# Kernel tuning notes

Hardware: AMD Instinct MI355X
Metric: run time of the kernel (lower is better)

Reference implementation:

```python
import jax, jax.numpy as jnp
import numpy as np

B, T, IN, D, H, L, OUT = 256, 100, 6, 1024, 8, 4, 256
HD = D // H
SCALE = 1.0 / float(np.sqrt(HD))


def _pe(t, d):
    # sinusoidal positional encoding [t, d]
    pos = np.arange(t, dtype=np.float32)[:, None]
    div = np.exp(np.arange(0, d, 2, dtype=np.float32) * (-np.log(10000.0) / d))
    pe = np.zeros((t, d), np.float32)
    pe[:, 0::2] = np.sin(pos * div)
    pe[:, 1::2] = np.cos(pos * div)
    return jnp.asarray(pe)


def _ln(x, g, b, eps=1e-5):
    m = x.mean(-1, keepdims=True)
    v = ((x - m) ** 2).mean(-1, keepdims=True)
    return (x - m) * jax.lax.rsqrt(v + eps) * g + b


def setup_inputs() -> dict:
    ks = jax.random.split(jax.random.key(0), 8)
    s = 0.02
    return {
        "x": jax.random.normal(ks[0], (B, T, IN), jnp.float32),
        "Wi": jax.random.normal(ks[1], (IN, D), jnp.float32) * s,
        "bi": jnp.zeros((D,), jnp.float32),
        "qkv_w": jax.random.normal(ks[2], (L, 3 * D, D), jnp.float32) * s,
        "qkv_b": jnp.zeros((L, 3 * D), jnp.float32),
        "out_w": jax.random.normal(ks[3], (L, D, D), jnp.float32) * s,
        "out_b": jnp.zeros((L, D), jnp.float32),
        "ff1_w": jax.random.normal(ks[4], (L, D, D), jnp.float32) * s,
        "ff1_b": jnp.zeros((L, D), jnp.float32),
        "ff2_w": jax.random.normal(ks[5], (L, D, D), jnp.float32) * s,
        "ff2_b": jnp.zeros((L, D), jnp.float32),
        "ln1_g": jnp.ones((L, D), jnp.float32),
        "ln1_b": jnp.zeros((L, D), jnp.float32),
        "ln2_g": jnp.ones((L, D), jnp.float32),
        "ln2_b": jnp.zeros((L, D), jnp.float32),
        "Wo": jax.random.normal(ks[6], (T * D, OUT), jnp.float32) * s,
        "bo": jnp.zeros((OUT,), jnp.float32),
    }


def reference(x, Wi, bi, qkv_w, qkv_b, out_w, out_b, ff1_w, ff1_b,
              ff2_w, ff2_b, ln1_g, ln1_b, ln2_g, ln2_b, Wo, bo):
    b, t, _ = x.shape
    # vectorized equivalent of the python double loop: mask[i, j, :] = 1 where x[i, j, 0] == 0
    row = (x[:, :, 0] == 0).astype(x.dtype)                    # [B, T]
    base = jnp.broadcast_to(row[:, :, None], (b, t, t))        # [B, T, T]
    # torch: mask.repeat(H,1,1).reshape(H*B, T, T); MHA batch slot (bi, h) reads flat b*H+h
    amask = jnp.tile(base, (H, 1, 1)).reshape(b, H, t, t)      # additive float mask (+1)

    h = x @ Wi + bi + _pe(t, D)[None, :, :]                     # [B, T, D] (dropout off at eval)

    for i in range(L):  # post-norm encoder layers, identical weights structure
        qkv = h @ qkv_w[i].T + qkv_b[i]
        q, k, v = jnp.split(qkv, 3, axis=-1)
        q = q.reshape(b, t, H, HD)
        k = k.reshape(b, t, H, HD)
        v = v.reshape(b, t, H, HD)
        scores = jnp.einsum('bqhd,bkhd->bhqk', q, k) * SCALE + amask
        attn = jax.nn.softmax(scores, axis=-1)
        ctx = jnp.einsum('bhqk,bkhd->bqhd', attn, v).reshape(b, t, D)
        h = _ln(h + ctx @ out_w[i].T + out_b[i], ln1_g[i], ln1_b[i])
        ff = jax.nn.relu(h @ ff1_w[i].T + ff1_b[i]) @ ff2_w[i].T + ff2_b[i]
        h = _ln(h + ff, ln2_g[i], ln2_b[i])

    return h.reshape(b, t * D) @ Wo + bo                        # [B, OUT]
```

## Files before the change

### kernel.cpp

```cpp
#include <hip/hip_runtime.h>


#define B_    256
#define T_    100
#define D_    1024
#define H_    8
#define HD_   128
#define L_    4
#define BT_   25600
#define DQ_   3072
#define OUT_  256
#define KFIN_ 102400
#define KSPLIT_ 32
#define SCALE_ 0.08838834764831845f

typedef unsigned short ushort_t;
typedef __attribute__((ext_vector_type(8))) short bf16x8;
typedef __attribute__((ext_vector_type(4))) float f32x4;

__device__ inline ushort_t f2bf(float f) {
  unsigned u = __float_as_uint(f);
  u += 0x7FFFu + ((u >> 16) & 1u);
  return (ushort_t)(u >> 16);
}
__device__ inline float bf2f(ushort_t u) {
  return __uint_as_float((unsigned)u << 16);
}

__device__ inline void gld16(const void* g, void* l) {
  __builtin_amdgcn_global_load_lds(
      (__attribute__((address_space(1))) unsigned int*)(size_t)g,
      (__attribute__((address_space(3))) unsigned int*)l, 16, 0, 0);
}

#define GBUF_ 65536
#define GBOF_ 32768

#define STAGE256(hs_) do { \
    const int hs__ = (hs_); \
    if (hs__ < 64) { \
      const int tt__ = hs__ >> 2, id__ = hs__ & 3; \
      const int half__ = id__ >> 1; \
      const int bo__ = (tt__ & 1) * GBUF_ + half__ * 16384 + wsl \
                     + ((id__ & 1) ? GBOF_ : 0); \
      const ushort_t* s__ = ((id__ & 1) ? gB : gA) \
                     + (size_t)(half__ * 128) * 1024 + tt__ * 64; \
      gld16(s__, lds + bo__); \
      gld16(s__ + 8 * 1024, lds + bo__ + 1024); \
    } \
  } while (0)

#define LDA256(Mi) do { \
    const char* ba__ = lds + ldsoff + (Mi) * 16384 + rbA; \
    _Pragma("unroll") for (int i_ = 0; i_ < 4; ++i_) { \
      aF[i_][0] = *(const bf16x8*)(ba__ + i_ * 2048 + c0); \
      aF[i_][1] = *(const bf16x8*)(ba__ + i_ * 2048 + c1); \
    } \
  } while (0)

#define LDB256(Ni, BF) do { \
    const char* bb__ = lds + ldsoff + (Ni) * 16384 + rbB; \
    _Pragma("unroll") for (int j_ = 0; j_ < 2; ++j_) { \
      BF[j_][0] = *(const bf16x8*)(bb__ + j_ * 2048 + c0); \
      BF[j_][1] = *(const bf16x8*)(bb__ + j_ * 2048 + c1); \
    } \
  } while (0)

#define MM256(Mi, Ni, BF) do { \
    _Pragma("unroll") for (int i_ = 0; i_ < 4; ++i_) \
      _Pragma("unroll") for (int j_ = 0; j_ < 2; ++j_) { \
        acc[Mi][Ni][i_][j_] = __builtin_amdgcn_mfma_f32_16x16x32_bf16( \
            aF[i_][0], BF[j_][0], acc[Mi][Ni][i_][j_], 0, 0, 0); \
        acc[Mi][Ni][i_][j_] = __builtin_amdgcn_mfma_f32_16x16x32_bf16( \
            aF[i_][1], BF[j_][1], acc[Mi][Ni][i_][j_], 0, 0, 0); \
      } \
  } while (0)

#define VM6_ asm volatile("s_waitcnt vmcnt(6)" ::: "memory")
#define VM0_ asm volatile("s_waitcnt vmcnt(0)" ::: "memory")

#define PH256(t, p, LOADS, Mi, Ni, BF, VM) do { \
    LOADS; \
    STAGE256(7 + 4 * (t) + (p)); \
    __builtin_amdgcn_s_barrier(); \
    asm volatile("s_waitcnt lgkmcnt(0)" ::: "memory"); \
    __builtin_amdgcn_sched_barrier(0); \
    __builtin_amdgcn_s_setprio(1); \
    MM256(Mi, Ni, BF); \
    __builtin_amdgcn_s_setprio(0); \
    VM; \
    __builtin_amdgcn_s_barrier(); \
  } while (0)

#define TILE256(t, VM) do { \
    const int ldsoff = ((t) & 1) * GBUF_; \
    PH256(t, 0, { LDA256(0); LDB256(0, bF0); }, 0, 0, bF0, (void)0); \
    PH256(t, 1, { LDB256(1, bF1); },            0, 1, bF1, (void)0); \
    PH256(t, 2, { LDA256(1); },                 1, 1, bF1, (void)0); \
    PH256(t, 3, { },                            1, 0, bF0, VM); \
  } while (0)

template<int RELU, int RESID>
__global__ __launch_bounds__(512, 1)
void gemm256(const ushort_t* __restrict__ A, const ushort_t* __restrict__ Bw,
             const float* __restrict__ bias,
             ushort_t* __restrict__ outb, const ushort_t* __restrict__ resid,
             int N)
{
  __shared__ char lds[131072];
  const int tid = threadIdx.x;
  const int lane = tid & 63, w = tid >> 6;
  const int fr = lane & 15, q = lane >> 4;
  const int wm = w >> 2, wn = w & 3;

  const int nwg = gridDim.x;
  const int nbx = N >> 8;
  const int qd = nwg >> 3, r8 = nwg & 7;
  const int xcd = blockIdx.x & 7, idx = blockIdx.x >> 3;
  const int wg = (xcd < r8 ? xcd * (qd + 1) : r8 * (qd + 1) + (xcd - r8) * qd) + idx;
  const int m0 = (wg / nbx) * 256, n0 = (wg % nbx) * 256;

  const int lr8 = lane >> 3;
  const int xch = (lane & 7) ^ lr8;
  const ushort_t* gA = A  + (size_t)(m0 + w * 16 + lr8) * 1024 + xch * 8;
  const ushort_t* gB = Bw + (size_t)(n0 + w * 16 + lr8) * 1024 + xch * 8;
  const int wsl = w * 2048;

  const int c0 = (q ^ (fr & 7)) * 16;
  const int c1 = ((4 + q) ^ (fr & 7)) * 16;
  const int rbA = (wm * 64 + fr) * 128;
  const int rbB = GBOF_ + (wn * 32 + fr) * 128;

  f32x4 acc[2][2][4][2];
  #pragma unroll
  for (int a0 = 0; a0 < 2; ++a0)
    #pragma unroll
    for (int a1 = 0; a1 < 2; ++a1)
      #pragma unroll
      for (int a2 = 0; a2 < 4; ++a2)
        #pragma unroll
        for (int a3 = 0; a3 < 2; ++a3) acc[a0][a1][a2][a3] = 0.f;
  bf16x8 aF[4][2], bF0[2][2], bF1[2][2];

  #pragma unroll
  for (int hs = 0; hs < 7; ++hs) STAGE256(hs);
  VM6_;
  __builtin_amdgcn_s_barrier();

  for (int tp = 0; tp < 7; ++tp) {
    TILE256(2 * tp,     VM6_);
    TILE256(2 * tp + 1, VM6_);
  }
  TILE256(14, VM0_);
  TILE256(15, (void)0);

  const int erow = lane >> 2;
  const int ecc  = lane & 3;
  char* wb = lds + w * 4096;
  float bvv[2][2];
  #pragma unroll
  for (int Ni = 0; Ni < 2; ++Ni)
    #pragma unroll
    for (int jn = 0; jn < 2; ++jn)
      bvv[Ni][jn] = bias ? bias[n0 + Ni * 128 + wn * 32 + jn * 16 + fr] : 0.f;

  #pragma unroll
  for (int Mi = 0; Mi < 2; ++Mi)
    #pragma unroll
    for (int Ni = 0; Ni < 2; ++Ni) {
      #pragma unroll
      for (int i = 0; i < 4; ++i)
        #pragma unroll
        for (int jn = 0; jn < 2; ++jn)
          #pragma unroll
          for (int rr = 0; rr < 4; ++rr) {
            const int row = i * 16 + q * 4 + rr;
            float v = acc[Mi][Ni][i][jn][rr] + bvv[Ni][jn];
            if (RELU) v = fmaxf(v, 0.f);
            const int cp = (jn * 2 + (fr >> 3)) ^ ((row >> 2) & 3);
            *(ushort_t*)(wb + row * 64 + cp * 16 + (fr & 7) * 2) = f2bf(v);
          }
      #pragma unroll
      for (int rd = 0; rd < 4; ++rd) {
        const int row = rd * 16 + erow;
        const int sc = ecc ^ ((row >> 2) & 3);
        bf16x8 seg = *(const bf16x8*)(wb + row * 64 + sc * 16);
        const size_t gaddr = (size_t)(m0 + Mi * 128 + wm * 64 + row) * N
                           + (n0 + Ni * 128 + wn * 32 + ecc * 8);
        if (RESID) {
          const bf16x8 rv = *(const bf16x8*)&resid[gaddr];
          #pragma unroll
          for (int e = 0; e < 8; ++e)
            seg[e] = (short)f2bf(bf2f((ushort_t)seg[e]) + bf2f((ushort_t)rv[e]));
        }
        *(bf16x8*)&outb[gaddr] = seg;
      }
    }
}

template<int RELU, int RESID, int OBF, int OF32>
__global__ __launch_bounds__(256)
void gemm_nt(const ushort_t* __restrict__ A, const ushort_t* __restrict__ Bw,
             const float* __restrict__ bias,
             ushort_t* outb, float* outf, const ushort_t* __restrict__ resid,
             int M, int N, int K, int ksteps)
{
  __shared__ ushort_t lds[16384];
  ushort_t* lsA = lds;
  ushort_t* lsB = lds + 8192;
  const int tid = threadIdx.x, lane = tid & 63, wave = tid >> 6;
  const int fr = lane & 15, q = lane >> 4;
  const int m0 = blockIdx.y * 128, n0 = blockIdx.x * 128;
  const int wm = (wave >> 1) * 64, wn = (wave & 1) * 64;
  const int kbase = blockIdx.z * ksteps * 64;

  const ushort_t* Ab = A + (size_t)m0 * K + kbase;
  const ushort_t* Bb = Bw + (size_t)n0 * K + kbase;

  const int kg = (lane & 7) ^ (lane >> 3);
  const ushort_t* gaA = Ab + (size_t)(lane >> 3) * K + kg * 8;
  const ushort_t* gaB = Bb + (size_t)(lane >> 3) * K + kg * 8;

  f32x4 acc[4][4];
  #pragma unroll
  for (int i = 0; i < 4; i++)
    #pragma unroll
    for (int j = 0; j < 4; j++) acc[i][j] = 0.f;

  int rowA[4], rowB[4];
  #pragma unroll
  for (int t = 0; t < 4; t++) {
    rowA[t] = (wm + t * 16 + fr) * 64;
    rowB[t] = (wn + t * 16 + fr) * 64;
  }
  const int sl0 = ((0 * 4 + q) ^ (fr & 7)) * 8;
  const int sl1 = ((1 * 4 + q) ^ (fr & 7)) * 8;

  for (int ks = 0; ks < ksteps; ks++) {
    __syncthreads();
    #pragma unroll
    for (int u = 0; u < 4; u++) {
      const int i = wave * 4 + u;
      gld16(gaA + ks * 64 + (size_t)i * 8 * K, lsA + i * 512);
      gld16(gaB + ks * 64 + (size_t)i * 8 * K, lsB + i * 512);
    }
    __syncthreads();
    #pragma unroll
    for (int s = 0; s < 2; s++) {
      const int sl = s ? sl1 : sl0;
      bf16x8 af[4], bfv[4];
      #pragma unroll
      for (int t = 0; t < 4; t++) {
        af[t]  = *(const bf16x8*)(lsA + rowA[t] + sl);
        bfv[t] = *(const bf16x8*)(lsB + rowB[t] + sl);
      }
      #pragma unroll
      for (int i = 0; i < 4; i++)
        #pragma unroll
        for (int j = 0; j < 4; j++)
          acc[i][j] = __builtin_amdgcn_mfma_f32_16x16x32_bf16(af[i], bfv[j], acc[i][j], 0, 0, 0);
    }
  }

  if (OBF) {
    __syncthreads();
    ushort_t* myl = lds + wave * 2048;
    const int rloc = lane >> 2, cg = lane & 3;
    #pragma unroll
    for (int hh = 0; hh < 2; hh++) {
      #pragma unroll
      for (int j2 = 0; j2 < 2; j2++) {
        const int j = 2 * hh + j2;
        const float bv = bias ? bias[n0 + wn + j * 16 + fr] : 0.f;
        #pragma unroll
        for (int i = 0; i < 4; i++) {
          #pragma unroll
          for (int rr = 0; rr < 4; rr++) {
            const int row = i * 16 + q * 4 + rr;
            const int col = j2 * 16 + fr;
            float v = acc[i][j][rr] + bv;
            if (RELU) v = fmaxf(v, 0.f);
            const int cgw = col >> 3, cwi = col & 7;
            myl[(row * 4 + (cgw ^ (row & 3) ^ ((row >> 2) & 3))) * 8 + cwi] = f2bf(v);
          }
        }
      }
      #pragma unroll
      for (int rb = 0; rb < 4; rb++) {
        const int row = rb * 16 + rloc;
        const int cgr = cg ^ (row & 3) ^ ((row >> 2) & 3);
        bf16x8 seg = *(const bf16x8*)&myl[(row * 4 + cgr) * 8];
        const size_t gaddr = (size_t)(m0 + wm + row) * N + (n0 + wn + hh * 32 + cg * 8);
        if (RESID) {
          const bf16x8 rv = *(const bf16x8*)&resid[gaddr];
          #pragma unroll
          for (int e = 0; e < 8; e++) {
            const float f = bf2f((ushort_t)seg[e]) + bf2f((ushort_t)rv[e]);
            seg[e] = (short)f2bf(f);
          }
        }
        *(bf16x8*)&outb[gaddr] = seg;
      }
    }
  }
  if (OF32) {
    float* po = outf + (size_t)blockIdx.z * M * N;
    #pragma unroll
    for (int i = 0; i < 4; i++) {
      const int rb = m0 + wm + i * 16 + q * 4;
      #pragma unroll
      for (int j = 0; j < 4; j++) {
        const int col = n0 + wn + j * 16 + fr;
        #pragma unroll
        for (int rr = 0; rr < 4; rr++)
          po[(size_t)(rb + rr) * N + col] = acc[i][j][rr];
      }
    }
  }
}

#define KST 136
#define VST 120
#define PST 120

__global__ __launch_bounds__(256)
void attn_kernel(const ushort_t* __restrict__ qkv, ushort_t* __restrict__ ctx)
{
  __shared__ ushort_t Kls[112 * KST];
  __shared__ ushort_t Vt[128 * VST];
  __shared__ ushort_t Pls[64 * PST];
  const int tid = threadIdx.x, lane = tid & 63, wave = tid >> 6;
  const int fr = lane & 15, q = lane >> 4;
  const int hh = blockIdx.x, bb = blockIdx.y;
  const size_t base = (size_t)bb * T_ * DQ_;
  const ushort_t* Qb = qkv + base + hh * HD_;
  const ushort_t* Kb = qkv + base + D_ + hh * HD_;
  const ushort_t* Vb = qkv + base + 2 * D_ + hh * HD_;

  for (int e = tid; e < 1600; e += 256) {
    const int j = e >> 4, kc = e & 15;
    *(bf16x8*)&Kls[j * KST + kc * 8] = *(const bf16x8*)(Kb + (size_t)j * DQ_ + kc * 8);
  }
  for (int e = tid; e < 12 * KST; e += 256) Kls[100 * KST + e] = 0;
  for (int e = tid; e < 1600; e += 256) {
    const int j = e >> 4, dc = e & 15;
    const bf16x8 v = *(const bf16x8*)(Vb + (size_t)j * DQ_ + dc * 8);
    #pragma unroll
    for (int u = 0; u < 8; u++) Vt[(dc * 8 + u) * VST + j] = (ushort_t)v[u];
  }
  for (int e = tid; e < 128 * 12; e += 256) {
    const int d = e / 12, j = e - d * 12;
    Vt[d * VST + 100 + j] = 0;
  }
  __syncthreads();

  for (int c = 0; c < 2; c++) {
    if (c) __syncthreads();
    const int it  = c * 4 + wave;
    const bool wlive = (it < 7);
    const int itc = wlive ? it : 6;
    const int qrow = min(itc * 16 + fr, T_ - 1);
    bf16x8 aq[4];
    #pragma unroll
    for (int ks = 0; ks < 4; ks++)
      aq[ks] = *(const bf16x8*)(Qb + (size_t)qrow * DQ_ + ks * 32 + q * 8);
    f32x4 sacc[7];
    #pragma unroll
    for (int jt = 0; jt < 7; jt++) sacc[jt] = 0.f;
    #pragma unroll
    for (int ks = 0; ks < 4; ks++) {
      const int kk = ks * 32 + q * 8;
      #pragma unroll
      for (int jt = 0; jt < 7; jt++) {
        const bf16x8 kb = *(const bf16x8*)&Kls[(jt * 16 + fr) * KST + kk];
        sacc[jt] = __builtin_amdgcn_mfma_f32_16x16x32_bf16(aq[ks], kb, sacc[jt], 0, 0, 0);
      }
    }
    ushort_t pbf[7][4];
    #pragma unroll
    for (int rr = 0; rr < 4; rr++) {
      float sv[7];
      float mx = -1e30f;
      #pragma unroll
      for (int jt = 0; jt < 7; jt++) {
        float s = sacc[jt][rr] * SCALE_;
        if (jt == 6 && fr >= 4) s = -1e30f;
        sv[jt] = s;
        mx = fmaxf(mx, s);
      }
      mx = fmaxf(mx, __shfl_xor(mx, 1));
      mx = fmaxf(mx, __shfl_xor(mx, 2));
      mx = fmaxf(mx, __shfl_xor(mx, 4));
      mx = fmaxf(mx, __shfl_xor(mx, 8));
      float sum = 0.f;
      #pragma unroll
      for (int jt = 0; jt < 7; jt++) { sv[jt] = __expf(sv[jt] - mx); sum += sv[jt]; }
      sum += __shfl_xor(sum, 1);
      sum += __shfl_xor(sum, 2);
      sum += __shfl_xor(sum, 4);
      sum += __shfl_xor(sum, 8);
      const float inv = 1.f / sum;
      #pragma unroll
      for (int jt = 0; jt < 7; jt++) pbf[jt][rr] = f2bf(sv[jt] * inv);
    }
    if (wlive) {
      #pragma unroll
      for (int jt = 0; jt < 7; jt++)
        #pragma unroll
        for (int rr = 0; rr < 4; rr++)
          Pls[(wave * 16 + q * 4 + rr) * PST + jt * 16 + fr] = pbf[jt][rr];
    }
    __syncthreads();
    const int mtc = (c == 0) ? 4 : 3;
    f32x4 cacc[4][2];
    #pragma unroll
    for (int i = 0; i < 4; i++) { cacc[i][0] = 0.f; cacc[i][1] = 0.f; }
    #pragma unroll
    for (int ks = 0; ks < 4; ks++) {
      const int kk = ks * 32 + q * 8;
      const bool live = (ks < 3) || (q < 2);
      bf16x8 v0 = 0, v1 = 0;
      if (live) {
        v0 = *(const bf16x8*)&Vt[((wave * 2 + 0) * 16 + fr) * VST + kk];
        v1 = *(const bf16x8*)&Vt[((wave * 2 + 1) * 16 + fr) * VST + kk];
      }
      for (int mt = 0; mt < mtc; mt++) {
        bf16x8 a = 0;
        if (live) a = *(const bf16x8*)&Pls[(mt * 16 + fr) * PST + kk];
        cacc[mt][0] = __builtin_amdgcn_mfma_f32_16x16x32_bf16(a, v0, cacc[mt][0], 0, 0, 0);
        cacc[mt][1] = __builtin_amdgcn_mfma_f32_16x16x32_bf16(a, v1, cacc[mt][1], 0, 0, 0);
      }
    }
    for (int mt = 0; mt < mtc; mt++) {
      #pragma unroll
      for (int nn = 0; nn < 2; nn++) {
        const int col = hh * HD_ + (wave * 2 + nn) * 16 + fr;
        #pragma unroll
        for (int rr = 0; rr < 4; rr++) {
          const int r = c * 64 + mt * 16 + q * 4 + rr;
          if (r < T_)
            ctx[(size_t)(bb * T_ + r) * D_ + col] = f2bf(cacc[mt][nn][rr]);
        }
      }
    }
  }
}

__global__ __launch_bounds__(256)
void ln_kernel(const ushort_t* __restrict__ in, ushort_t* __restrict__ outb,
               const float* __restrict__ g, const float* __restrict__ bta)
{
  const int row = blockIdx.x, tid = threadIdx.x;
  const int c4 = tid * 4;
  const ushort4 uv = *(const ushort4*)(in + (size_t)row * D_ + c4);
  const float v0 = bf2f(uv.x), v1 = bf2f(uv.y), v2 = bf2f(uv.z), v3 = bf2f(uv.w);
  float s  = v0 + v1 + v2 + v3;
  float ss = v0*v0 + v1*v1 + v2*v2 + v3*v3;
  #pragma unroll
  for (int o = 1; o < 64; o <<= 1) {
    s  += __shfl_xor(s, o);
    ss += __shfl_xor(ss, o);
  }
  __shared__ float red[8];
  const int lane = tid & 63, wave = tid >> 6;
  if (lane == 0) { red[wave] = s; red[4 + wave] = ss; }
  __syncthreads();
  s  = red[0] + red[1] + red[2] + red[3];
  ss = red[4] + red[5] + red[6] + red[7];
  const float mean = s * (1.f / D_);
  const float var  = ss * (1.f / D_) - mean * mean;
  const float rstd = rsqrtf(var + 1e-5f);
  const float4 gv = *(const float4*)(g + c4);
  const float4 bv = *(const float4*)(bta + c4);
  ushort4 ob = { f2bf((v0 - mean) * rstd * gv.x + bv.x),
                 f2bf((v1 - mean) * rstd * gv.y + bv.y),
                 f2bf((v2 - mean) * rstd * gv.z + bv.z),
                 f2bf((v3 - mean) * rstd * gv.w + bv.w) };
  *(ushort4*)(outb + (size_t)row * D_ + c4) = ob;
}

__global__ __launch_bounds__(256)
void pe_init(float* __restrict__ pe)
{
  const int t = blockIdx.x;
  #pragma unroll
  for (int j = 0; j < 2; ++j) {
    const int k = threadIdx.x + j * 256;
    const float ang = (float)t * expf((float)k * -0.017988946039015984f);
    float s, c;
    sincosf(ang, &s, &c);
    pe[t * D_ + 2 * k]     = s;
    pe[t * D_ + 2 * k + 1] = c;
  }
}

__global__ __launch_bounds__(256)
void embed_kernel(const float* __restrict__ x, const float* __restrict__ Wi,
                  const float* __restrict__ bi, const float* __restrict__ pe,
                  ushort_t* __restrict__ hbf)
{
  const int row = blockIdx.x;
  const int t = row % T_;
  const int c = threadIdx.x * 4;
  float xv[6];
  #pragma unroll
  for (int i = 0; i < 6; i++) xv[i] = x[row * 6 + i];
  const float4 pv = *(const float4*)(pe + t * D_ + c);
  const float4 bv = *(const float4*)(bi + c);
  float a0 = bv.x + pv.x, a1 = bv.y + pv.y, a2 = bv.z + pv.z, a3 = bv.w + pv.w;
  #pragma unroll
  for (int i = 0; i < 6; i++) {
    const float4 wv = *(const float4*)(Wi + i * D_ + c);
    a0 += xv[i] * wv.x; a1 += xv[i] * wv.y;
    a2 += xv[i] * wv.z; a3 += xv[i] * wv.w;
  }
  ushort4 ob = { f2bf(a0), f2bf(a1), f2bf(a2), f2bf(a3) };
  *(ushort4*)(hbf + (size_t)row * D_ + c) = ob;
}

#define NQW (L_*DQ_*D_)
#define NDW (L_*D_*D_)
__global__ void cvt_all(const float* __restrict__ qw, const float* __restrict__ ow,
                        const float* __restrict__ f1, const float* __restrict__ f2,
                        ushort_t* wq, ushort_t* wo, ushort_t* w1, ushort_t* w2)
{
  const size_t i = ((size_t)blockIdx.x * 256 + threadIdx.x) * 4;
  const float* s; ushort_t* d; size_t off;
  if (i < NQW)                { s = qw; d = wq; off = i; }
  else if (i < NQW + NDW)     { s = ow; d = wo; off = i - NQW; }
  else if (i < NQW + 2*NDW)   { s = f1; d = w1; off = i - NQW - NDW; }
  else                        { s = f2; d = w2; off = i - NQW - 2*NDW; }
  const float4 v = *(const float4*)(s + off);
  ushort4 o = { f2bf(v.x), f2bf(v.y), f2bf(v.z), f2bf(v.w) };
  *(ushort4*)(d + off) = o;
}

__global__ __launch_bounds__(256)
void transpose_wo(const float* __restrict__ src, ushort_t* __restrict__ dst)
{
  __shared__ float tile[64][65];
  const int k0 = blockIdx.x * 64, n0 = blockIdx.y * 64;
  const int tc = threadIdx.x & 63, tr = threadIdx.x >> 6;
  #pragma unroll
  for (int i = 0; i < 16; i++) {
    const int r = i * 4 + tr;
    tile[r][tc] = src[(size_t)(k0 + r) * OUT_ + n0 + tc];
  }
  __syncthreads();
  #pragma unroll
  for (int i = 0; i < 16; i++) {
    const int n = i * 4 + tr;
    dst[(size_t)(n0 + n) * KFIN_ + k0 + tc] = f2bf(tile[tc][n]);
  }
}

__global__ void reduce_final(const float* __restrict__ part,
                             const float* __restrict__ bo, float* __restrict__ out)
{
  const int i = blockIdx.x * 256 + threadIdx.x;
  float s = bo[i & (OUT_ - 1)];
  for (int z = 0; z < KSPLIT_; z++) s += part[(size_t)z * OUT_ * OUT_ + i];
  out[i] = s;
}

extern "C" void kernel_launch(void* const* d_in, const int* in_sizes, int n_in,
                              void* d_out, int out_size, void* d_ws, size_t ws_size,
                              hipStream_t stream)
{
  (void)in_sizes; (void)n_in; (void)out_size; (void)ws_size;
  const float* x     = (const float*)d_in[0];
  const float* Wi    = (const float*)d_in[1];
  const float* bi    = (const float*)d_in[2];
  const float* qkv_w = (const float*)d_in[3];
  const float* qkv_b = (const float*)d_in[4];
  const float* out_w = (const float*)d_in[5];
  const float* out_b = (const float*)d_in[6];
  const float* ff1_w = (const float*)d_in[7];
  const float* ff1_b = (const float*)d_in[8];
  const float* ff2_w = (const float*)d_in[9];
  const float* ff2_b = (const float*)d_in[10];
  const float* ln1_g = (const float*)d_in[11];
  const float* ln1_b = (const float*)d_in[12];
  const float* ln2_g = (const float*)d_in[13];
  const float* ln2_b = (const float*)d_in[14];
  const float* Wo    = (const float*)d_in[15];
  const float* bo    = (const float*)d_in[16];
  float* out = (float*)d_out;

  char* p = (char*)d_ws;
  ushort_t* hbf  = (ushort_t*)p; p += (size_t)BT_ * D_ * 2;
  ushort_t* qkvb = (ushort_t*)p; p += (size_t)BT_ * DQ_ * 2;
  ushort_t* ctxb = (ushort_t*)p; p += (size_t)BT_ * D_ * 2;
  ushort_t* wq   = (ushort_t*)p; p += (size_t)NQW * 2;
  ushort_t* wo   = (ushort_t*)p; p += (size_t)NDW * 2;
  ushort_t* w1   = (ushort_t*)p; p += (size_t)NDW * 2;
  ushort_t* w2   = (ushort_t*)p; p += (size_t)NDW * 2;
  float*    pe   = (float*)p;    p += (size_t)T_ * D_ * 4;
  ushort_t* ffact = qkvb;
  ushort_t* sum   = qkvb + (size_t)BT_ * D_;
  ushort_t* wot   = ctxb;
  float*    part  = (float*)qkvb;

  cvt_all<<<dim3((NQW + 3*NDW) / 1024), 256, 0, stream>>>(
      qkv_w, out_w, ff1_w, ff2_w, wq, wo, w1, w2);
  pe_init<<<dim3(T_), 256, 0, stream>>>(pe);
  embed_kernel<<<dim3(BT_), 256, 0, stream>>>(x, Wi, bi, pe, hbf);

  for (int i = 0; i < L_; i++) {
    gemm256<0,0><<<dim3((BT_/256)*(DQ_/256)), 512, 0, stream>>>(
        hbf, wq + (size_t)i * DQ_ * D_, qkv_b + i * DQ_, qkvb, nullptr, DQ_);
    attn_kernel<<<dim3(H_, B_), 256, 0, stream>>>(qkvb, ctxb);
    gemm256<0,1><<<dim3((BT_/256)*(D_/256)), 512, 0, stream>>>(
        ctxb, wo + (size_t)i * D_ * D_, out_b + i * D_, sum, hbf, D_);
    ln_kernel<<<dim3(BT_), 256, 0, stream>>>(sum, hbf, ln1_g + i * D_, ln1_b + i * D_);
    gemm256<1,0><<<dim3((BT_/256)*(D_/256)), 512, 0, stream>>>(
        hbf, w1 + (size_t)i * D_ * D_, ff1_b + i * D_, ffact, nullptr, D_);
    gemm256<0,1><<<dim3((BT_/256)*(D_/256)), 512, 0, stream>>>(
        ffact, w2 + (size_t)i * D_ * D_, ff2_b + i * D_, sum, hbf, D_);
    ln_kernel<<<dim3(BT_), 256, 0, stream>>>(sum, hbf, ln2_g + i * D_, ln2_b + i * D_);
  }

  transpose_wo<<<dim3(KFIN_/64, OUT_/64), 256, 0, stream>>>(Wo, wot);
  gemm_nt<0,0,0,1><<<dim3(OUT_/128, OUT_/128, KSPLIT_), 256, 0, stream>>>(
      hbf, wot, nullptr, nullptr, part, nullptr,
      OUT_, OUT_, KFIN_, KFIN_ / (KSPLIT_ * 64));
  reduce_final<<<dim3(OUT_ * OUT_ / 256), 256, 0, stream>>>(part, bo, out);
}
```

Baseline: 2.373 ms.

## Add 128x256 double-buffered GEMM for D-by-D layers and unroll attention loops

Adds a new gemm128 kernel with 128x256 output tiles, a double-buffered LDS pipeline, XCD-aware block remapping and an occupancy hint of four workgroups. It replaces the 256x256 GEMM for the out-projection, FF1 and FF2 layers. For N=1024 the larger tiles gave only 400 workgroups, and the smaller tiles give 800, which spreads the work more evenly over the compute units. The attention kernel's PV and store loops are also fully unrolled with predication. The dead OBF epilogue is removed from gemm_nt. The risks are less data reuse per tile and heavier register pressure.

```diff
diff --git a/kernel.cpp b/kernel.cpp
--- a/kernel.cpp
+++ b/kernel.cpp
@@ -32,6 +32,12 @@
       (__attribute__((address_space(1))) unsigned int*)(size_t)g,
       (__attribute__((address_space(3))) unsigned int*)l, 16, 0, 0);
 }
+
+#define MFMA_(a, b, c) __builtin_amdgcn_mfma_f32_16x16x32_bf16(a, b, c, 0, 0, 0)
+
+#define VM6_ asm volatile("s_waitcnt vmcnt(6)" ::: "memory")
+#define VM3_ asm volatile("s_waitcnt vmcnt(3)" ::: "memory")
+#define VM0_ asm volatile("s_waitcnt vmcnt(0)" ::: "memory")
 
 #define GBUF_ 65536
 #define GBOF_ 32768
@@ -69,15 +75,10 @@
 #define MM256(Mi, Ni, BF) do { \
     _Pragma("unroll") for (int i_ = 0; i_ < 4; ++i_) \
       _Pragma("unroll") for (int j_ = 0; j_ < 2; ++j_) { \
-        acc[Mi][Ni][i_][j_] = __builtin_amdgcn_mfma_f32_16x16x32_bf16( \
-            aF[i_][0], BF[j_][0], acc[Mi][Ni][i_][j_], 0, 0, 0); \
-        acc[Mi][Ni][i_][j_] = __builtin_amdgcn_mfma_f32_16x16x32_bf16( \
-            aF[i_][1], BF[j_][1], acc[Mi][Ni][i_][j_], 0, 0, 0); \
+        acc[Mi][Ni][i_][j_] = MFMA_(aF[i_][0], BF[j_][0], acc[Mi][Ni][i_][j_]); \
+        acc[Mi][Ni][i_][j_] = MFMA_(aF[i_][1], BF[j_][1], acc[Mi][Ni][i_][j_]); \
       } \
   } while (0)
-
-#define VM6_ asm volatile("s_waitcnt vmcnt(6)" ::: "memory")
-#define VM0_ asm volatile("s_waitcnt vmcnt(0)" ::: "memory")
 
 #define PH256(t, p, LOADS, Mi, Ni, BF, VM) do { \
     LOADS; \
@@ -198,6 +199,132 @@
     }
 }
 
+#define LBUF_ 24576
+
+#define STG(t_) do { \
+    const int lo__ = ((t_) & 1) * LBUF_; \
+    gld16(gA  + (t_) * 32, lds + lo__ + dA); \
+    gld16(gB0 + (t_) * 32, lds + lo__ + dB0); \
+    gld16(gB1 + (t_) * 32, lds + lo__ + dB0 + 1024); \
+  } while (0)
+
+#define TIL(t_, STAGES_, VMW_) do { \
+    const int lo_ = ((t_) & 1) * LBUF_; \
+    _Pragma("unroll") for (int i_ = 0; i_ < 4; ++i_) \
+      aF[i_] = *(const bf16x8*)(lds + lo_ + rbA + i_ * 1024 + cR); \
+    _Pragma("unroll") for (int j_ = 0; j_ < 4; ++j_) \
+      bF[j_] = *(const bf16x8*)(lds + lo_ + rbB + j_ * 1024 + cR); \
+    asm volatile("s_waitcnt lgkmcnt(0)" ::: "memory"); \
+    __builtin_amdgcn_sched_barrier(0); \
+    __builtin_amdgcn_s_setprio(1); \
+    _Pragma("unroll") for (int i_ = 0; i_ < 4; ++i_) { \
+      acc[i_][0] = MFMA_(aF[i_], bF[0], acc[i_][0]); \
+      acc[i_][1] = MFMA_(aF[i_], bF[1], acc[i_][1]); } \
+    __builtin_amdgcn_s_setprio(0); \
+    __builtin_amdgcn_s_barrier(); \
+    __builtin_amdgcn_sched_barrier(0); \
+    STAGES_; \
+    __builtin_amdgcn_s_setprio(1); \
+    _Pragma("unroll") for (int i_ = 0; i_ < 4; ++i_) { \
+      acc[i_][2] = MFMA_(aF[i_], bF[2], acc[i_][2]); \
+      acc[i_][3] = MFMA_(aF[i_], bF[3], acc[i_][3]); } \
+    __builtin_amdgcn_s_setprio(0); \
+    VMW_; \
+    __builtin_amdgcn_s_barrier(); \
+    __builtin_amdgcn_sched_barrier(0); \
+  } while (0)
+
+template<int RELU, int RESID>
+__global__ __launch_bounds__(512, 4)
+void gemm128(const ushort_t* __restrict__ A, const ushort_t* __restrict__ Bw,
+             const float* __restrict__ bias,
+             ushort_t* __restrict__ outb, const ushort_t* __restrict__ resid,
+             int N)
+{
+  __shared__ __align__(16) char lds[49152];
+  const int tid = threadIdx.x;
+  const int lane = tid & 63, w = tid >> 6;
+  const int fr = lane & 15, q = lane >> 4;
+  const int wm = w >> 2, wn = w & 3;
+
+  const int nwg = gridDim.x;
+  const int nbx = N >> 8;
+  const int qd = nwg >> 3, r8 = nwg & 7;
+  const int xcd = blockIdx.x & 7, idx = blockIdx.x >> 3;
+  const int wg = (xcd < r8 ? xcd * (qd + 1) : r8 * (qd + 1) + (xcd - r8) * qd) + idx;
+  const int m0 = (wg / nbx) * 128, n0 = (wg % nbx) * 256;
+
+  const int xc = (lane & 3) ^ ((lane >> 3) & 3);
+  const ushort_t* gA  = A  + (size_t)(m0 + w * 16 + (lane >> 2)) * 1024 + xc * 8;
+  const ushort_t* gB0 = Bw + (size_t)(n0 + w * 32 + (lane >> 2)) * 1024 + xc * 8;
+  const ushort_t* gB1 = gB0 + 16 * 1024;
+  const int dA  = w * 1024;
+  const int dB0 = 8192 + w * 2048;
+
+  const int cR  = fr * 64 + ((q ^ ((fr >> 1) & 3)) << 4);
+  const int rbA = wm * 4096;
+  const int rbB = 8192 + wn * 4096;
+
+  f32x4 acc[4][4];
+  #pragma unroll
+  for (int i = 0; i < 4; ++i)
+    #pragma unroll
+    for (int j = 0; j < 4; ++j) acc[i][j] = 0.f;
+  bf16x8 aF[4], bF[4];
+
+  STG(0); STG(1);
+  VM3_;
+  __builtin_amdgcn_s_barrier();
+  __builtin_amdgcn_sched_barrier(0);
+
+  #pragma unroll
+  for (int t = 0; t < 30; ++t) TIL(t, STG(t + 2), VM3_);
+  TIL(30, (void)0, VM0_);
+  TIL(31, (void)0, (void)0);
+  __syncthreads();
+
+  const int erow = lane >> 2;
+  const int ecc  = lane & 3;
+  char* wb = lds + w * 4096;
+  float bvv[2][2];
+  #pragma unroll
+  for (int jh = 0; jh < 2; ++jh)
+    #pragma unroll
+    for (int jn = 0; jn < 2; ++jn)
+      bvv[jh][jn] = bias ? bias[n0 + wn * 64 + jh * 32 + jn * 16 + fr] : 0.f;
+
+  #pragma unroll
+  for (int jh = 0; jh < 2; ++jh) {
+    #pragma unroll
+    for (int i = 0; i < 4; ++i)
+      #pragma unroll
+      for (int jn = 0; jn < 2; ++jn)
+        #pragma unroll
+        for (int rr = 0; rr < 4; ++rr) {
+          const int row = i * 16 + q * 4 + rr;
+          float v = acc[i][jh * 2 + jn][rr] + bvv[jh][jn];
+          if (RELU) v = fmaxf(v, 0.f);
+          const int cp = (jn * 2 + (fr >> 3)) ^ ((row >> 2) & 3);
+          *(ushort_t*)(wb + row * 64 + cp * 16 + (fr & 7) * 2) = f2bf(v);
+        }
+    #pragma unroll
+    for (int rd = 0; rd < 4; ++rd) {
+      const int row = rd * 16 + erow;
+      const int sc = ecc ^ ((row >> 2) & 3);
+      bf16x8 seg = *(const bf16x8*)(wb + row * 64 + sc * 16);
+      const size_t gaddr = (size_t)(m0 + wm * 64 + row) * N
+                         + (n0 + wn * 64 + jh * 32 + ecc * 8);
+      if (RESID) {
+        const bf16x8 rv = *(const bf16x8*)&resid[gaddr];
+        #pragma unroll
+        for (int e = 0; e < 8; ++e)
+          seg[e] = (short)f2bf(bf2f((ushort_t)seg[e]) + bf2f((ushort_t)rv[e]));
+      }
+      *(bf16x8*)&outb[gaddr] = seg;
+    }
+  }
+}
+
 template<int RELU, int RESID, int OBF, int OF32>
 __global__ __launch_bounds__(256)
 void gemm_nt(const ushort_t* __restrict__ A, const ushort_t* __restrict__ Bw,
@@ -258,51 +385,10 @@
       for (int i = 0; i < 4; i++)
         #pragma unroll
         for (int j = 0; j < 4; j++)
-          acc[i][j] = __builtin_amdgcn_mfma_f32_16x16x32_bf16(af[i], bfv[j], acc[i][j], 0, 0, 0);
-    }
-  }
-
-  if (OBF) {
-    __syncthreads();
-    ushort_t* myl = lds + wave * 2048;
-    const int rloc = lane >> 2, cg = lane & 3;
-    #pragma unroll
-    for (int hh = 0; hh < 2; hh++) {
-      #pragma unroll
-      for (int j2 = 0; j2 < 2; j2++) {
-        const int j = 2 * hh + j2;
-        const float bv = bias ? bias[n0 + wn + j * 16 + fr] : 0.f;
-        #pragma unroll
-        for (int i = 0; i < 4; i++) {
-          #pragma unroll
-          for (int rr = 0; rr < 4; rr++) {
-            const int row = i * 16 + q * 4 + rr;
-            const int col = j2 * 16 + fr;
-            float v = acc[i][j][rr] + bv;
-            if (RELU) v = fmaxf(v, 0.f);
-            const int cgw = col >> 3, cwi = col & 7;
-            myl[(row * 4 + (cgw ^ (row & 3) ^ ((row >> 2) & 3))) * 8 + cwi] = f2bf(v);
-          }
-        }
-      }
-      #pragma unroll
-      for (int rb = 0; rb < 4; rb++) {
-        const int row = rb * 16 + rloc;
-        const int cgr = cg ^ (row & 3) ^ ((row >> 2) & 3);
-        bf16x8 seg = *(const bf16x8*)&myl[(row * 4 + cgr) * 8];
-        const size_t gaddr = (size_t)(m0 + wm + row) * N + (n0 + wn + hh * 32 + cg * 8);
-        if (RESID) {
-          const bf16x8 rv = *(const bf16x8*)&resid[gaddr];
-          #pragma unroll
-          for (int e = 0; e < 8; e++) {
-            const float f = bf2f((ushort_t)seg[e]) + bf2f((ushort_t)rv[e]);
-            seg[e] = (short)f2bf(f);
-          }
-        }
-        *(bf16x8*)&outb[gaddr] = seg;
-      }
-    }
-  }
+          acc[i][j] = MFMA_(af[i], bfv[j], acc[i][j]);
+    }
+  }
+
   if (OF32) {
     float* po = outf + (size_t)blockIdx.z * M * N;
     #pragma unroll
@@ -354,6 +440,7 @@
   }
   __syncthreads();
 
+  #pragma unroll
   for (int c = 0; c < 2; c++) {
     if (c) __syncthreads();
     const int it  = c * 4 + wave;
@@ -373,7 +460,7 @@
       #pragma unroll
       for (int jt = 0; jt < 7; jt++) {
         const bf16x8 kb = *(const bf16x8*)&Kls[(jt * 16 + fr) * KST + kk];
-        sacc[jt] = __builtin_amdgcn_mfma_f32_16x16x32_bf16(aq[ks], kb, sacc[jt], 0, 0, 0);
+        sacc[jt] = MFMA_(aq[ks], kb, sacc[jt]);
       }
     }
     ushort_t pbf[7][4];
@@ -424,22 +511,28 @@
         v0 = *(const bf16x8*)&Vt[((wave * 2 + 0) * 16 + fr) * VST + kk];
         v1 = *(const bf16x8*)&Vt[((wave * 2 + 1) * 16 + fr) * VST + kk];
       }
-      for (int mt = 0; mt < mtc; mt++) {
-        bf16x8 a = 0;
-        if (live) a = *(const bf16x8*)&Pls[(mt * 16 + fr) * PST + kk];
-        cacc[mt][0] = __builtin_amdgcn_mfma_f32_16x16x32_bf16(a, v0, cacc[mt][0], 0, 0, 0);
-        cacc[mt][1] = __builtin_amdgcn_mfma_f32_16x16x32_bf16(a, v1, cacc[mt][1], 0, 0, 0);
-      }
-    }
-    for (int mt = 0; mt < mtc; mt++) {
-      #pragma unroll
-      for (int nn = 0; nn < 2; nn++) {
-        const int col = hh * HD_ + (wave * 2 + nn) * 16 + fr;
+      #pragma unroll
+      for (int mt = 0; mt < 4; mt++) {
+        if (mt < mtc) {
+          bf16x8 a = 0;
+          if (live) a = *(const bf16x8*)&Pls[(mt * 16 + fr) * PST + kk];
+          cacc[mt][0] = MFMA_(a, v0, cacc[mt][0]);
+          cacc[mt][1] = MFMA_(a, v1, cacc[mt][1]);
+        }
+      }
+    }
+    #pragma unroll
+    for (int mt = 0; mt < 4; mt++) {
+      if (mt < mtc) {
         #pragma unroll
-        for (int rr = 0; rr < 4; rr++) {
-          const int r = c * 64 + mt * 16 + q * 4 + rr;
-          if (r < T_)
-            ctx[(size_t)(bb * T_ + r) * D_ + col] = f2bf(cacc[mt][nn][rr]);
+        for (int nn = 0; nn < 2; nn++) {
+          const int col = hh * HD_ + (wave * 2 + nn) * 16 + fr;
+          #pragma unroll
+          for (int rr = 0; rr < 4; rr++) {
+            const int r = c * 64 + mt * 16 + q * 4 + rr;
+            if (r < T_)
+              ctx[(size_t)(bb * T_ + r) * D_ + col] = f2bf(cacc[mt][nn][rr]);
+          }
         }
       }
     }
@@ -610,12 +703,12 @@
     gemm256<0,0><<<dim3((BT_/256)*(DQ_/256)), 512, 0, stream>>>(
         hbf, wq + (size_t)i * DQ_ * D_, qkv_b + i * DQ_, qkvb, nullptr, DQ_);
     attn_kernel<<<dim3(H_, B_), 256, 0, stream>>>(qkvb, ctxb);
-    gemm256<0,1><<<dim3((BT_/256)*(D_/256)), 512, 0, stream>>>(
+    gemm128<0,1><<<dim3((BT_/128)*(D_/256)), 512, 0, stream>>>(
         ctxb, wo + (size_t)i * D_ * D_, out_b + i * D_, sum, hbf, D_);
     ln_kernel<<<dim3(BT_), 256, 0, stream>>>(sum, hbf, ln1_g + i * D_, ln1_b + i * D_);
-    gemm256<1,0><<<dim3((BT_/256)*(D_/256)), 512, 0, stream>>>(
+    gemm128<1,0><<<dim3((BT_/128)*(D_/256)), 512, 0, stream>>>(
         hbf, w1 + (size_t)i * D_ * D_, ff1_b + i * D_, ffact, nullptr, D_);
-    gemm256<0,1><<<dim3((BT_/256)*(D_/256)), 512, 0, stream>>>(
+    gemm128<0,1><<<dim3((BT_/128)*(D_/256)), 512, 0, stream>>>(
         ffact, w2 + (size_t)i * D_ * D_, ff2_b + i * D_, sum, hbf, D_);
     ln_kernel<<<dim3(BT_), 256, 0, stream>>>(sum, hbf, ln2_g + i * D_, ln2_b + i * D_);
   }
```

Measured after the change: 2.200 ms. 7.3% less time.
